# Optimization experiments

Measured on AMD Instinct MI355X. Metric: run time of the kernel, lower is better.

The kernel has to match this reference:

```python
import jax, jax.numpy as jnp
import numpy as np

B, GRID, C, K = 8, 24, 768, 3          # batch, ViT patch grid, embed dim, PatchMaker patchsize
PRE_DIM, TGT_DIM = 1024, 1024          # pretrain_embed_dimension, target_embed_dimension
N_MEM, IMG = 20000, 384                # coreset memory bank size, input image size


def adaptive_avg_pool_matrix(lin, lout):
    """Dense matrix M (lout, lin) so that x @ M.T == F.adaptive_avg_pool1d(x, lout)."""
    M = np.zeros((lout, lin), dtype=np.float32)
    for i in range(lout):
        s = (i * lin) // lout
        e = -(((-(i + 1)) * lin) // lout)  # ceil((i+1)*lin/lout)
        M[i, s:e] = 1.0 / (e - s)
    return jnp.asarray(M)


def unfold3x3(x):
    """torch.nn.Unfold(kernel=3, stride=1, pad=1): (B,C,H,W) -> (B, H*W, C, 3, 3)."""
    b, c, h, w = x.shape
    xp = jnp.pad(x, ((0, 0), (0, 0), (1, 1), (1, 1)))
    # stack shifted views in torch Unfold's (C, kh, kw) channel-major order
    p = jnp.stack([xp[:, :, i:i + h, j:j + w] for i in range(K) for j in range(K)], axis=2)
    p = p.reshape(b, c, K, K, h * w).transpose(0, 4, 1, 2, 3)
    return p


def setup_inputs() -> dict:
    key = jax.random.key(0)
    k1, k2, k3, k4 = jax.random.split(key, 4)
    return {
        "feats6": jax.random.normal(k1, (B, GRID * GRID + 1, C), jnp.float32),
        "feats8": jax.random.normal(k2, (B, GRID * GRID + 1, C), jnp.float32),
        "feats10": jax.random.normal(k3, (B, GRID * GRID + 1, C), jnp.float32),
        "memory_bank": jax.random.normal(k4, (N_MEM, TGT_DIM), jnp.float32),
    }


def reference(feats6, feats8, feats10, memory_bank):
    Mpre = adaptive_avg_pool_matrix(C * K * K, PRE_DIM)   # MeanMapper pooling
    Magg = adaptive_avg_pool_matrix(3 * PRE_DIM, TGT_DIM)  # Aggregator pooling

    pooled = []
    for f in (feats6, feats8, feats10):
        # drop CLS token, reshape to CNN-like grid (B, C, 24, 24)
        g = f[:, 1:, :].reshape(B, GRID, GRID, C).transpose(0, 3, 1, 2)
        # patchify (all layers share the 24x24 grid, so the bilinear re-alignment
        # to ref_num_patches in the original code is an identity here)
        p = unfold3x3(g).reshape(B * GRID * GRID, C * K * K)
        pooled.append(p @ Mpre.T)                         # (N, PRE_DIM)
    feats = jnp.stack(pooled, axis=1).reshape(-1, 3 * PRE_DIM)
    emb = feats @ Magg.T                                  # (N, TGT_DIM)

    # squared-L2 nearest neighbour against coreset memory bank (FaissNN IndexFlatL2)
    d2 = (jnp.sum(emb * emb, axis=1, keepdims=True)
          + jnp.sum(memory_bank * memory_bank, axis=1)[None, :]
          - 2.0 * emb @ memory_bank.T)                    # (N, N_MEM)
    patch_scores = jnp.min(d2, axis=1)                    # anomaly_score_num_nn = 1

    ps = patch_scores.reshape(B, GRID, GRID)
    image_scores = jnp.max(ps.reshape(B, -1), axis=1)     # PatchMaker.score (max over patches)
    masks = jax.image.resize(ps, (B, IMG, IMG), method="bilinear")  # RescaleSegmentor
    return image_scores, masks
```

## Files before the change

kernel.cpp:

```cpp
#include <hip/hip_runtime.h>
#include <hip/hip_bf16.h>
#include <stdint.h>

#define B_      8
#define GRID_   24
#define C_      768
#define NPATCH  (B_*GRID_*GRID_)
#define PRE     1024
#define TGT     1024
#define NMEM    20000
#define NMEM_PAD 20096
#define IMG_    384
#define SEQ     577

typedef __bf16 bf16_t;
typedef bf16_t bf16x8 __attribute__((ext_vector_type(8)));
typedef bf16_t bf16x4 __attribute__((ext_vector_type(4)));
typedef float  floatx4 __attribute__((ext_vector_type(4)));

__global__ __launch_bounds__(256) void emb_kernel(
    const float* __restrict__ f6, const float* __restrict__ f8,
    const float* __restrict__ f10,
    bf16_t* __restrict__ emb, float* __restrict__ enorm)
{
    __shared__ float pooled[3*PRE];
    __shared__ float red[4];

    const int n   = blockIdx.x;
    const int b   = n / (GRID_*GRID_);
    const int yx  = n - b*(GRID_*GRID_);
    const int y   = yx / GRID_;
    const int x   = yx - y*GRID_;
    const int t   = threadIdx.x;

    const float* fl[3] = {f6, f8, f10};

#pragma unroll
    for (int l = 0; l < 3; ++l) {
        const float* f = fl[l];
        float A0 = 0.f, B0 = 0.f, C1 = 0.f, D1 = 0.f, E2 = 0.f, F2 = 0.f;
#pragma unroll
        for (int k = 0; k < 9; ++k) {
            const int kh = k / 3, kw = k - kh*3;
            const int ny = y + kh - 1, nx = x + kw - 1;
            const bool v = (ny >= 0 && ny < GRID_ && nx >= 0 && nx < GRID_);
            const int off = v ? (b*SEQ + 1 + ny*GRID_ + nx) : (b*SEQ);
            const float* p = f + (size_t)off*C_ + 3*t;
            float a = p[0], bq = p[1], c = p[2];
            if (!v) { a = 0.f; bq = 0.f; c = 0.f; }
            if (k <= 6) A0 += a;
            if (k >= 6) B0 += a;
            if (k <= 4) C1 += bq;
            if (k >= 4) D1 += bq;
            if (k <= 2) E2 += c;
            if (k >= 2) F2 += c;
        }
        float4 pv;
        pv.x = A0 * (1.f/7.f);
        pv.y = (B0 + C1) * (1.f/8.f);
        pv.z = (D1 + E2) * (1.f/8.f);
        pv.w = F2 * (1.f/7.f);
        *(float4*)(pooled + l*PRE + 4*t) = pv;
    }
    __syncthreads();

    float psq = 0.f;
    bf16x4 ev;
#pragma unroll
    for (int r = 0; r < 4; ++r) {
        const int j = 4*t + r;
        float vv = (pooled[3*j] + pooled[3*j+1] + pooled[3*j+2]) * (1.f/3.f);
        ev[r] = (bf16_t)vv;
        psq += vv*vv;
    }
    *(bf16x4*)(emb + (size_t)n*TGT + 4*t) = ev;

    for (int off = 32; off > 0; off >>= 1) psq += __shfl_down(psq, off, 64);
    if ((t & 63) == 0) red[t >> 6] = psq;
    __syncthreads();
    if (t == 0) enorm[n] = (red[0] + red[1]) + (red[2] + red[3]);
}

__global__ __launch_bounds__(256) void mprep_kernel(
    const float* __restrict__ mb, bf16_t* __restrict__ mbf,
    float* __restrict__ mnorm)
{
    const int r = blockIdx.x;
    const int t = threadIdx.x;
    __shared__ float red[4];
    float psq = 0.f;
    if (r < NMEM) {
        float4 v = ((const float4*)(mb + (size_t)r*TGT))[t];
        bf16x4 o;
        o[0] = (bf16_t)v.x; o[1] = (bf16_t)v.y;
        o[2] = (bf16_t)v.z; o[3] = (bf16_t)v.w;
        ((bf16x4*)(mbf + (size_t)r*TGT))[t] = o;
        psq = v.x*v.x + v.y*v.y + v.z*v.z + v.w*v.w;
    } else {
        bf16x4 z; z[0] = z[1] = z[2] = z[3] = (bf16_t)0.f;
        ((bf16x4*)(mbf + (size_t)r*TGT))[t] = z;
    }
    for (int off = 32; off > 0; off >>= 1) psq += __shfl_down(psq, off, 64);
    if ((t & 63) == 0) red[t >> 6] = psq;
    __syncthreads();
    if (t == 0) mnorm[r] = (r < NMEM) ? ((red[0]+red[1])+(red[2]+red[3])) : 1e30f;
}

__global__ void init_kernel(int* __restrict__ p)
{
    int i = blockIdx.x*256 + threadIdx.x;
    if (i < NPATCH) p[i] = 0x7f7f7f7f;
}

__device__ __forceinline__ void load_lds16(const void* g, void* l)
{
    __builtin_amdgcn_global_load_lds(
        (__attribute__((address_space(1))) void*)g,
        (__attribute__((address_space(3))) void*)l, 16, 0, 0);
}

__global__ __launch_bounds__(256) void nnmin_kernel(
    const bf16_t* __restrict__ E, const bf16_t* __restrict__ M,
    const float* __restrict__ enorm, const float* __restrict__ mnorm,
    int* __restrict__ out_min)
{
    __shared__ __attribute__((aligned(16))) bf16_t As[128*32];
    __shared__ __attribute__((aligned(16))) bf16_t Bs[128*32];

    const int m0   = blockIdx.x * 128;
    const int n0   = blockIdx.y * 128;
    const int tid  = threadIdx.x;
    const int wave = tid >> 6;
    const int lane = tid & 63;
    const int wm   = wave >> 1;
    const int wn   = wave & 1;

    const int sr   = lane >> 2;
    const int slot = lane & 3;
    const int kg   = slot ^ ((sr >> 1) & 3);

    const bf16_t* gA0 = E + (size_t)(m0 + wave*16 + sr)*TGT + kg*8;
    const bf16_t* gA1 = gA0 + (size_t)64*TGT;
    const bf16_t* gB0 = M + (size_t)(n0 + wave*16 + sr)*TGT + kg*8;
    const bf16_t* gB1 = gB0 + (size_t)64*TGT;
    bf16_t* lA0 = As + wave*512 + lane*8;
    bf16_t* lA1 = lA0 + 64*32;
    bf16_t* lB0 = Bs + wave*512 + lane*8;
    bf16_t* lB1 = lB0 + 64*32;

    floatx4 acc[4][4];
#pragma unroll
    for (int i = 0; i < 4; ++i)
#pragma unroll
        for (int j = 0; j < 4; ++j) acc[i][j] = (floatx4)0.0f;

    const int fr = lane & 15;
    const int fg = lane >> 4;
    const int sg = fg ^ ((fr >> 1) & 3);

    for (int k0 = 0; k0 < TGT; k0 += 32) {
        load_lds16(gA0 + k0, lA0);
        load_lds16(gA1 + k0, lA1);
        load_lds16(gB0 + k0, lB0);
        load_lds16(gB1 + k0, lB1);
        __syncthreads();

        bf16x8 a[4], b[4];
#pragma unroll
        for (int t = 0; t < 4; ++t)
            a[t] = *(const bf16x8*)(As + (wm*64 + t*16 + fr)*32 + sg*8);
#pragma unroll
        for (int t = 0; t < 4; ++t)
            b[t] = *(const bf16x8*)(Bs + (wn*64 + t*16 + fr)*32 + sg*8);
#pragma unroll
        for (int tm = 0; tm < 4; ++tm)
#pragma unroll
            for (int tn = 0; tn < 4; ++tn)
                acc[tm][tn] = __builtin_amdgcn_mfma_f32_16x16x32_bf16(
                    a[tm], b[tn], acc[tm][tn], 0, 0, 0);
        __syncthreads();
    }

    const int col  = lane & 15;
    const int rowq = (lane >> 4) * 4;
    const int colbase = n0 + wn*64;
#pragma unroll
    for (int tm = 0; tm < 4; ++tm) {
#pragma unroll
        for (int r = 0; r < 4; ++r) {
            int row = m0 + wm*64 + tm*16 + rowq + r;
            float en = enorm[row];
            float best = 1e38f;
#pragma unroll
            for (int tn = 0; tn < 4; ++tn) {
                float d2 = en + mnorm[colbase + tn*16 + col]
                         - 2.0f * acc[tm][tn][r];
                best = fminf(best, d2);
            }
#pragma unroll
            for (int off = 1; off < 16; off <<= 1)
                best = fminf(best, __shfl_xor(best, off, 64));
            if (col == 0)
                atomicMin(&out_min[row], __float_as_int(best));
        }
    }
}

__global__ __launch_bounds__(256) void score_kernel(
    const int* __restrict__ ps_bits, float* __restrict__ out)
{
    const int b = blockIdx.x, tid = threadIdx.x;
    __shared__ float red[4];
    float m = -1e38f;
    for (int i = tid; i < GRID_*GRID_; i += 256)
        m = fmaxf(m, __int_as_float(ps_bits[b*GRID_*GRID_ + i]));
    for (int off = 32; off > 0; off >>= 1) m = fmaxf(m, __shfl_down(m, off, 64));
    if ((tid & 63) == 0) red[tid >> 6] = m;
    __syncthreads();
    if (tid == 0) out[b] = fmaxf(fmaxf(red[0], red[1]), fmaxf(red[2], red[3]));
}

__global__ __launch_bounds__(256) void mask_kernel(
    const int* __restrict__ ps_bits, float* __restrict__ masks)
{
    int idx = blockIdx.x*256 + threadIdx.x;
    int b  = idx / (IMG_*IMG_);
    int p  = idx - b*(IMG_*IMG_);
    int oy = p / IMG_, ox = p - oy*IMG_;

    float fy = (oy + 0.5f) * (1.0f/16.0f) - 0.5f;
    float fx = (ox + 0.5f) * (1.0f/16.0f) - 0.5f;
    int y0 = (int)floorf(fy); float ty = fy - (float)y0;
    int x0 = (int)floorf(fx); float tx = fx - (float)x0;
    int y0c = min(max(y0, 0), GRID_-1), y1c = min(max(y0+1, 0), GRID_-1);
    int x0c = min(max(x0, 0), GRID_-1), x1c = min(max(x0+1, 0), GRID_-1);

    const int* psb = ps_bits + b*GRID_*GRID_;
    float v00 = __int_as_float(psb[y0c*GRID_ + x0c]);
    float v01 = __int_as_float(psb[y0c*GRID_ + x1c]);
    float v10 = __int_as_float(psb[y1c*GRID_ + x0c]);
    float v11 = __int_as_float(psb[y1c*GRID_ + x1c]);
    float v0 = v00 + (v01 - v00)*tx;
    float v1 = v10 + (v11 - v10)*tx;
    masks[idx] = v0 + (v1 - v0)*ty;
}

extern "C" void kernel_launch(void* const* d_in, const int* in_sizes, int n_in,
                              void* d_out, int out_size, void* d_ws, size_t ws_size,
                              hipStream_t stream)
{
    const float* f6  = (const float*)d_in[0];
    const float* f8  = (const float*)d_in[1];
    const float* f10 = (const float*)d_in[2];
    const float* mb  = (const float*)d_in[3];
    float* out = (float*)d_out;

    char* ws = (char*)d_ws;
    bf16_t* emb  = (bf16_t*)ws;  ws += (size_t)NPATCH*TGT*sizeof(bf16_t);
    bf16_t* mbf  = (bf16_t*)ws;  ws += (size_t)NMEM_PAD*TGT*sizeof(bf16_t);
    float* enorm = (float*)ws;   ws += (size_t)NPATCH*sizeof(float);
    float* mnorm = (float*)ws;   ws += (size_t)NMEM_PAD*sizeof(float);
    int* psbits  = (int*)ws;     ws += (size_t)NPATCH*sizeof(int);

    hipLaunchKernelGGL(emb_kernel, dim3(NPATCH), dim3(256), 0, stream,
                       f6, f8, f10, emb, enorm);
    hipLaunchKernelGGL(mprep_kernel, dim3(NMEM_PAD), dim3(256), 0, stream,
                       mb, mbf, mnorm);
    hipLaunchKernelGGL(init_kernel, dim3((NPATCH+255)/256), dim3(256), 0, stream,
                       psbits);
    hipLaunchKernelGGL(nnmin_kernel, dim3(NPATCH/128, NMEM_PAD/128), dim3(256),
                       0, stream, emb, mbf, enorm, mnorm, psbits);
    hipLaunchKernelGGL(score_kernel, dim3(B_), dim3(256), 0, stream,
                       psbits, out);
    hipLaunchKernelGGL(mask_kernel, dim3((B_*IMG_*IMG_)/256), dim3(256), 0, stream,
                       psbits, out + B_);
}
```

Measured before the change: 443.7 us.

## Switch nearest-neighbour GEMM from bf16 to fp8 e4m3 scaled MFMA

Quantizes embeddings and the memory bank to fp8 e4m3 instead of bf16 and uses the 16x16x128 f8f6f4 scaled MFMA with K-tile 128 and a new LDS swizzle. Norms are computed from the dequantized values so distances stay consistent with the quantized dot products. The init kernel is folded into emb_kernel, and mprep now handles one row per wave. This halves GEMM operand bytes and doubles MFMA throughput, but fp8 precision may move the min distances beyond tolerance.

```diff
diff --git a/kernel.cpp b/kernel.cpp
--- a/kernel.cpp
+++ b/kernel.cpp
@@ -1,5 +1,6 @@
 #include <hip/hip_runtime.h>
 #include <hip/hip_bf16.h>
+#include <hip/hip_fp8.h>
 #include <stdint.h>
 
 #define B_      8
@@ -13,15 +14,15 @@
 #define IMG_    384
 #define SEQ     577
 
-typedef __bf16 bf16_t;
-typedef bf16_t bf16x8 __attribute__((ext_vector_type(8)));
-typedef bf16_t bf16x4 __attribute__((ext_vector_type(4)));
-typedef float  floatx4 __attribute__((ext_vector_type(4)));
+typedef int   intx4  __attribute__((ext_vector_type(4)));
+typedef int   intx8  __attribute__((ext_vector_type(8)));
+typedef float floatx4 __attribute__((ext_vector_type(4)));
 
 __global__ __launch_bounds__(256) void emb_kernel(
     const float* __restrict__ f6, const float* __restrict__ f8,
     const float* __restrict__ f10,
-    bf16_t* __restrict__ emb, float* __restrict__ enorm)
+    uint8_t* __restrict__ emb, float* __restrict__ enorm,
+    int* __restrict__ psbits)
 {
     __shared__ float pooled[3*PRE];
     __shared__ float red[4];
@@ -32,6 +33,8 @@
     const int y   = yx / GRID_;
     const int x   = yx - y*GRID_;
     const int t   = threadIdx.x;
+
+    if (t == 0) psbits[n] = 0x7f7f7f7f;
 
     const float* fl[3] = {f6, f8, f10};
 
@@ -65,15 +68,17 @@
     __syncthreads();
 
     float psq = 0.f;
-    bf16x4 ev;
+    unsigned ob = 0;
 #pragma unroll
     for (int r = 0; r < 4; ++r) {
         const int j = 4*t + r;
         float vv = (pooled[3*j] + pooled[3*j+1] + pooled[3*j+2]) * (1.f/3.f);
-        ev[r] = (bf16_t)vv;
-        psq += vv*vv;
-    }
-    *(bf16x4*)(emb + (size_t)n*TGT + 4*t) = ev;
+        __hip_fp8_e4m3 q(vv);
+        ob |= ((unsigned)q.__x) << (8*r);
+        float dq = (float)q;
+        psq += dq*dq;
+    }
+    *(unsigned*)(emb + (size_t)n*TGT + 4*t) = ob;
 
     for (int off = 32; off > 0; off >>= 1) psq += __shfl_down(psq, off, 64);
     if ((t & 63) == 0) red[t >> 6] = psq;
@@ -82,34 +87,32 @@
 }
 
 __global__ __launch_bounds__(256) void mprep_kernel(
-    const float* __restrict__ mb, bf16_t* __restrict__ mbf,
+    const float* __restrict__ mb, uint8_t* __restrict__ mq,
     float* __restrict__ mnorm)
 {
-    const int r = blockIdx.x;
-    const int t = threadIdx.x;
-    __shared__ float red[4];
+    const int r = blockIdx.x*4 + (threadIdx.x >> 6);
+    const int l = threadIdx.x & 63;
     float psq = 0.f;
+    unsigned ow[4];
     if (r < NMEM) {
-        float4 v = ((const float4*)(mb + (size_t)r*TGT))[t];
-        bf16x4 o;
-        o[0] = (bf16_t)v.x; o[1] = (bf16_t)v.y;
-        o[2] = (bf16_t)v.z; o[3] = (bf16_t)v.w;
-        ((bf16x4*)(mbf + (size_t)r*TGT))[t] = o;
-        psq = v.x*v.x + v.y*v.y + v.z*v.z + v.w*v.w;
+        const float4* src = (const float4*)(mb + (size_t)r*TGT) + l*4;
+#pragma unroll
+        for (int i = 0; i < 4; ++i) {
+            float4 v = src[i];
+            __hip_fp8_e4m3 q0(v.x), q1(v.y), q2(v.z), q3(v.w);
+            ow[i] = (unsigned)q0.__x | ((unsigned)q1.__x << 8)
+                  | ((unsigned)q2.__x << 16) | ((unsigned)q3.__x << 24);
+            float d0 = (float)q0, d1 = (float)q1, d2 = (float)q2, d3 = (float)q3;
+            psq += d0*d0 + d1*d1 + d2*d2 + d3*d3;
+        }
     } else {
-        bf16x4 z; z[0] = z[1] = z[2] = z[3] = (bf16_t)0.f;
-        ((bf16x4*)(mbf + (size_t)r*TGT))[t] = z;
-    }
+        ow[0] = ow[1] = ow[2] = ow[3] = 0u;
+    }
+    uint4 o4 = make_uint4(ow[0], ow[1], ow[2], ow[3]);
+    *(uint4*)(mq + (size_t)r*TGT + l*16) = o4;
+
     for (int off = 32; off > 0; off >>= 1) psq += __shfl_down(psq, off, 64);
-    if ((t & 63) == 0) red[t >> 6] = psq;
-    __syncthreads();
-    if (t == 0) mnorm[r] = (r < NMEM) ? ((red[0]+red[1])+(red[2]+red[3])) : 1e30f;
-}
-
-__global__ void init_kernel(int* __restrict__ p)
-{
-    int i = blockIdx.x*256 + threadIdx.x;
-    if (i < NPATCH) p[i] = 0x7f7f7f7f;
+    if (l == 0) mnorm[r] = (r < NMEM) ? psq : 1e30f;
 }
 
 __device__ __forceinline__ void load_lds16(const void* g, void* l)
@@ -119,13 +122,24 @@
         (__attribute__((address_space(3))) void*)l, 16, 0, 0);
 }
 
+__device__ __forceinline__ intx8 read_frag(const uint8_t* base, int row, int g)
+{
+    const int s0 = (2*g) ^ (row & 7);
+    const intx4 lo = *(const intx4*)(base + row*128 + s0*16);
+    const intx4 hi = *(const intx4*)(base + row*128 + (s0^1)*16);
+    intx8 r;
+    r[0]=lo[0]; r[1]=lo[1]; r[2]=lo[2]; r[3]=lo[3];
+    r[4]=hi[0]; r[5]=hi[1]; r[6]=hi[2]; r[7]=hi[3];
+    return r;
+}
+
 __global__ __launch_bounds__(256) void nnmin_kernel(
-    const bf16_t* __restrict__ E, const bf16_t* __restrict__ M,
+    const uint8_t* __restrict__ E, const uint8_t* __restrict__ M,
     const float* __restrict__ enorm, const float* __restrict__ mnorm,
     int* __restrict__ out_min)
 {
-    __shared__ __attribute__((aligned(16))) bf16_t As[128*32];
-    __shared__ __attribute__((aligned(16))) bf16_t Bs[128*32];
+    __shared__ __attribute__((aligned(16))) uint8_t As[128*128];
+    __shared__ __attribute__((aligned(16))) uint8_t Bs[128*128];
 
     const int m0   = blockIdx.x * 128;
     const int n0   = blockIdx.y * 128;
@@ -135,18 +149,12 @@
     const int wm   = wave >> 1;
     const int wn   = wave & 1;
 
-    const int sr   = lane >> 2;
-    const int slot = lane & 3;
-    const int kg   = slot ^ ((sr >> 1) & 3);
-
-    const bf16_t* gA0 = E + (size_t)(m0 + wave*16 + sr)*TGT + kg*8;
-    const bf16_t* gA1 = gA0 + (size_t)64*TGT;
-    const bf16_t* gB0 = M + (size_t)(n0 + wave*16 + sr)*TGT + kg*8;
-    const bf16_t* gB1 = gB0 + (size_t)64*TGT;
-    bf16_t* lA0 = As + wave*512 + lane*8;
-    bf16_t* lA1 = lA0 + 64*32;
-    bf16_t* lB0 = Bs + wave*512 + lane*8;
-    bf16_t* lB1 = lB0 + 64*32;
+    const int sr8 = lane >> 3;
+    const int sch = ((lane & 7) ^ sr8) * 16;
+    const uint8_t* gA = E + (size_t)(m0 + wave*8 + sr8)*TGT + sch;
+    const uint8_t* gB = M + (size_t)(n0 + wave*8 + sr8)*TGT + sch;
+    uint8_t* lA = As + wave*8*128 + lane*16;
+    uint8_t* lB = Bs + wave*8*128 + lane*16;
 
     floatx4 acc[4][4];
 #pragma unroll
@@ -156,28 +164,31 @@
 
     const int fr = lane & 15;
     const int fg = lane >> 4;
-    const int sg = fg ^ ((fr >> 1) & 3);
-
-    for (int k0 = 0; k0 < TGT; k0 += 32) {
-        load_lds16(gA0 + k0, lA0);
-        load_lds16(gA1 + k0, lA1);
-        load_lds16(gB0 + k0, lB0);
-        load_lds16(gB1 + k0, lB1);
+
+    for (int k0 = 0; k0 < TGT; k0 += 128) {
+#pragma unroll
+        for (int q = 0; q < 4; ++q) {
+            load_lds16(gA + (size_t)q*32*TGT + k0, lA + q*32*128);
+            load_lds16(gB + (size_t)q*32*TGT + k0, lB + q*32*128);
+        }
         __syncthreads();
 
-        bf16x8 a[4], b[4];
+        intx8 a[4], b[4];
 #pragma unroll
         for (int t = 0; t < 4; ++t)
-            a[t] = *(const bf16x8*)(As + (wm*64 + t*16 + fr)*32 + sg*8);
+            a[t] = read_frag(As, wm*64 + t*16 + fr, fg);
 #pragma unroll
         for (int t = 0; t < 4; ++t)
-            b[t] = *(const bf16x8*)(Bs + (wn*64 + t*16 + fr)*32 + sg*8);
+            b[t] = read_frag(Bs, wn*64 + t*16 + fr, fg);
 #pragma unroll
         for (int tm = 0; tm < 4; ++tm)
 #pragma unroll
             for (int tn = 0; tn < 4; ++tn)
-                acc[tm][tn] = __builtin_amdgcn_mfma_f32_16x16x32_bf16(
-                    a[tm], b[tn], acc[tm][tn], 0, 0, 0);
+                acc[tm][tn] = __builtin_amdgcn_mfma_scale_f32_16x16x128_f8f6f4(
+                    a[tm], b[tn], acc[tm][tn],
+                    0 , 0 ,
+                    0, 0x7f7f7f7f ,
+                    0, 0x7f7f7f7f );
         __syncthreads();
     }
 
@@ -256,20 +267,18 @@
     float* out = (float*)d_out;
 
     char* ws = (char*)d_ws;
-    bf16_t* emb  = (bf16_t*)ws;  ws += (size_t)NPATCH*TGT*sizeof(bf16_t);
-    bf16_t* mbf  = (bf16_t*)ws;  ws += (size_t)NMEM_PAD*TGT*sizeof(bf16_t);
+    uint8_t* emb = (uint8_t*)ws; ws += (size_t)NPATCH*TGT;
+    uint8_t* mq  = (uint8_t*)ws; ws += (size_t)NMEM_PAD*TGT;
     float* enorm = (float*)ws;   ws += (size_t)NPATCH*sizeof(float);
     float* mnorm = (float*)ws;   ws += (size_t)NMEM_PAD*sizeof(float);
     int* psbits  = (int*)ws;     ws += (size_t)NPATCH*sizeof(int);
 
     hipLaunchKernelGGL(emb_kernel, dim3(NPATCH), dim3(256), 0, stream,
-                       f6, f8, f10, emb, enorm);
-    hipLaunchKernelGGL(mprep_kernel, dim3(NMEM_PAD), dim3(256), 0, stream,
-                       mb, mbf, mnorm);
-    hipLaunchKernelGGL(init_kernel, dim3((NPATCH+255)/256), dim3(256), 0, stream,
-                       psbits);
+                       f6, f8, f10, emb, enorm, psbits);
+    hipLaunchKernelGGL(mprep_kernel, dim3(NMEM_PAD/4), dim3(256), 0, stream,
+                       mb, mq, mnorm);
     hipLaunchKernelGGL(nnmin_kernel, dim3(NPATCH/128, NMEM_PAD/128), dim3(256),
-                       0, stream, emb, mbf, enorm, mnorm, psbits);
+                       0, stream, emb, mq, enorm, mnorm, psbits);
     hipLaunchKernelGGL(score_kernel, dim3(B_), dim3(256), 0, stream,
                        psbits, out);
     hipLaunchKernelGGL(mask_kernel, dim3((B_*IMG_*IMG_)/256), dim3(256), 0, stream,
```

New measurement: 506.3 us. 14.1% more time.
